# Performance work log

Measured on AMD Instinct MI355X. Metric: run time of the kernel, lower is better.

## Reference

```python
import jax, jax.numpy as jnp
import numpy as np

B, L, D, H, K_DELAYS = 8, 2048, 512, 8, 8
DH = D // H


def setup_inputs() -> dict:
    key = jax.random.key(0)
    ks = jax.random.split(key, 6)
    def lin_w(k):
        return 0.02 * jax.random.normal(k, (D, D), jnp.float32)
    return {
        "x_q":  jax.random.normal(ks[0], (B, L, D), jnp.float32),
        "x_kv": jax.random.normal(ks[1], (B, L, D), jnp.float32),
        "Wq": lin_w(ks[2]), "bq": jnp.zeros((D,), jnp.float32),
        "Wk": lin_w(ks[3]), "bk": jnp.zeros((D,), jnp.float32),
        "Wv": lin_w(ks[4]), "bv": jnp.zeros((D,), jnp.float32),
        "Wo": lin_w(ks[5]), "bo": jnp.zeros((D,), jnp.float32),
    }


def reference(x_q, x_kv, Wq, bq, Wk, bk, Wv, bv, Wo, bo):
    Bx, Lx, Dx = x_q.shape

    def proj(x, W, b):  # torch Linear: x @ W.T + b, then split heads -> [B,H,L,dh]
        return (x @ W.T + b).reshape(Bx, Lx, H, DH).transpose(0, 2, 1, 3)

    q = proj(x_q, Wq, bq)
    k = proj(x_kv, Wk, bk)
    v = proj(x_kv, Wv, bv)

    # FFT-based autocorrelation over the time axis (axis=2)
    qz = q - q.mean(axis=2, keepdims=True)
    kz = k - k.mean(axis=2, keepdims=True)
    Qf = jnp.fft.rfft(qz, axis=2)
    Kf = jnp.fft.rfft(kz, axis=2)
    corr = jnp.fft.irfft(Qf * jnp.conj(Kf), n=Lx, axis=2).mean(axis=-1)  # [B,H,L]
    # torch expands corr to [B,H,Lq,Lk] then means over Lq -> identical to corr
    score = corr

    K = min(K_DELAYS, Lx)
    vals, idx = jax.lax.top_k(score, K)                    # [B,H,K]
    w = vals / (vals.sum(axis=-1, keepdims=True) + 1e-12)
    w = jax.lax.stop_gradient(w)                           # .detach() in torch

    # circular shift by -delay == gather at (t + delay) mod L
    t = jnp.arange(Lx)
    pos = (t[None, None, None, :] + idx[..., None]) % Lx   # [B,H,K,L]
    v_sh = jnp.take_along_axis(v[:, :, None, :, :], pos[..., None], axis=3)  # [B,H,K,L,dh]
    out = jnp.einsum('bhk,bhkld->bhld', w, v_sh)           # weighted sum over delays

    out = out.transpose(0, 2, 1, 3).reshape(Bx, Lx, Dx)
    return out @ Wo.T + bo
```

## Files before the change

### kernel.cpp

```cpp
#include <hip/hip_runtime.h>
#include <math.h>

#define BB 8
#define LL 2048
#define DD 512
#define HH 8
#define DHH 64
#define KD 8
#define MM (BB*LL)

typedef _Float16 f16x2 __attribute__((ext_vector_type(2)));
typedef _Float16 f16x4 __attribute__((ext_vector_type(4)));
typedef _Float16 f16x8 __attribute__((ext_vector_type(8)));
typedef float    f32x4 __attribute__((ext_vector_type(4)));

__device__ inline void cvt8(const float* __restrict__ s, _Float16* hp, _Float16* lp) {
    const float4 a = *(const float4*)s;
    const float4 b = *(const float4*)(s + 4);
    const float v[8] = {a.x, a.y, a.z, a.w, b.x, b.y, b.z, b.w};
    f16x8 hi, lo;
#pragma unroll
    for (int j = 0; j < 8; j++) {
        const _Float16 h = (_Float16)v[j];
        hi[j] = h;
        lo[j] = (_Float16)((v[j] - (float)h) * 512.0f);
    }
    *(f16x8*)hp = hi;
    if (lp) *(f16x8*)lp = lo;
}

__global__ __launch_bounds__(256) void prep_x(const float* __restrict__ xq,
                                              const float* __restrict__ xkv,
                                              _Float16* __restrict__ Xq_h, _Float16* __restrict__ Xq_l,
                                              _Float16* __restrict__ Xkv_h, _Float16* __restrict__ Xkv_l) {
    const int g = blockIdx.x * 256 + threadIdx.x;
    const int which = g >> 20;
    const size_t idx = (size_t)(g & 1048575) * 8;
    const float* src = which ? xkv : xq;
    _Float16* dh = which ? Xkv_h : Xq_h;
    _Float16* dl = which ? Xkv_l : Xq_l;
    cvt8(src + idx, dh + idx, dl + idx);
}

__global__ __launch_bounds__(256) void prep_w(const float* __restrict__ Wq, const float* __restrict__ Wk,
                                              const float* __restrict__ Wv, const float* __restrict__ Wo,
                                              _Float16* __restrict__ Wq_h, _Float16* __restrict__ Wq_l,
                                              _Float16* __restrict__ Wk_h, _Float16* __restrict__ Wk_l,
                                              _Float16* __restrict__ Wv_h, _Float16* __restrict__ Wo_h) {
    const int g = blockIdx.x * 256 + threadIdx.x;
    const int which = g >> 15;
    const size_t idx = (size_t)(g & 32767) * 8;
    if (which == 0)      cvt8(Wq + idx, Wq_h + idx, Wq_l + idx);
    else if (which == 1) cvt8(Wk + idx, Wk_h + idx, Wk_l + idx);
    else if (which == 2) cvt8(Wv + idx, Wv_h + idx, nullptr);
    else                 cvt8(Wo + idx, Wo_h + idx, nullptr);
}

template<int NPROD, int MODE>
__global__ __launch_bounds__(256, 2) void gemm_f16(const _Float16* __restrict__ Ag,
                                                   const _Float16* __restrict__ Al_g,
                                                   const _Float16* __restrict__ Bg,
                                                   const _Float16* __restrict__ Bl_g,
                                                   const float* __restrict__ bias,
                                                   void* __restrict__ Cv) {
    __shared__ __align__(16) _Float16 lds[(NPROD == 3) ? 20480 : 10240];
    _Float16* Ah = lds;
    _Float16* Bh = lds + 5120;
    _Float16* Al = (NPROD == 3) ? lds + 10240 : lds;
    _Float16* Bl = (NPROD == 3) ? lds + 15360 : lds;

    const int t  = threadIdx.x;
    const int l0 = blockIdx.x;
    const int m0 = (((l0 >> 5) << 3) | (l0 & 7)) * 128;
    const int n0 = ((l0 >> 3) & 3) * 128;

    const int lrow = t >> 2;
    const int lcol = (t & 3) * 8;
    const int wave = t >> 6;
    const int lane = t & 63;
    const int wm   = (wave >> 1) * 64;
    const int wn   = (wave & 1) * 64;
    const int lm   = lane & 15;
    const int quad = lane >> 4;

    f32x4 acc0[4][4] = {};
    f32x4 acc1[4][4] = {};

    f16x8 pa[2], pb[2], pal[2], pbl[2];
#pragma unroll
    for (int p = 0; p < 2; p++) {
        pa[p] = *(const f16x8*)(Ag + (size_t)(m0 + p * 64 + lrow) * 512 + lcol);
        pb[p] = *(const f16x8*)(Bg + (size_t)(n0 + p * 64 + lrow) * 512 + lcol);
        if (NPROD == 3) {
            pal[p] = *(const f16x8*)(Al_g + (size_t)(m0 + p * 64 + lrow) * 512 + lcol);
            pbl[p] = *(const f16x8*)(Bl_g + (size_t)(n0 + p * 64 + lrow) * 512 + lcol);
        }
    }

    for (int k0 = 0; k0 < 512; k0 += 32) {
        __syncthreads();
#pragma unroll
        for (int p = 0; p < 2; p++) {
            const int row = p * 64 + lrow;
            *(f16x8*)&Ah[row * 40 + lcol] = pa[p];
            *(f16x8*)&Bh[row * 40 + lcol] = pb[p];
            if (NPROD == 3) {
                *(f16x8*)&Al[row * 40 + lcol] = pal[p];
                *(f16x8*)&Bl[row * 40 + lcol] = pbl[p];
            }
        }
        __syncthreads();

        if (k0 + 32 < 512) {
            const int kn = k0 + 32;
#pragma unroll
            for (int p = 0; p < 2; p++) {
                pa[p] = *(const f16x8*)(Ag + (size_t)(m0 + p * 64 + lrow) * 512 + kn + lcol);
                pb[p] = *(const f16x8*)(Bg + (size_t)(n0 + p * 64 + lrow) * 512 + kn + lcol);
                if (NPROD == 3) {
                    pal[p] = *(const f16x8*)(Al_g + (size_t)(m0 + p * 64 + lrow) * 512 + kn + lcol);
                    pbl[p] = *(const f16x8*)(Bl_g + (size_t)(n0 + p * 64 + lrow) * 512 + kn + lcol);
                }
            }
        }

        f16x8 afh[4], bf[4];
#pragma unroll
        for (int mt = 0; mt < 4; mt++)
            afh[mt] = *(f16x8*)&Ah[(wm + mt * 16 + lm) * 40 + quad * 8];
#pragma unroll
        for (int nt = 0; nt < 4; nt++)
            bf[nt] = *(f16x8*)&Bh[(wn + nt * 16 + lm) * 40 + quad * 8];

#pragma unroll
        for (int mt = 0; mt < 4; mt++)
#pragma unroll
            for (int nt = 0; nt < 4; nt++)
                acc0[mt][nt] = __builtin_amdgcn_mfma_f32_16x16x32_f16(afh[mt], bf[nt], acc0[mt][nt], 0, 0, 0);

        if (NPROD == 3) {
            f16x8 afl[4];
#pragma unroll
            for (int mt = 0; mt < 4; mt++)
                afl[mt] = *(f16x8*)&Al[(wm + mt * 16 + lm) * 40 + quad * 8];
#pragma unroll
            for (int mt = 0; mt < 4; mt++)
#pragma unroll
                for (int nt = 0; nt < 4; nt++)
                    acc1[mt][nt] = __builtin_amdgcn_mfma_f32_16x16x32_f16(afl[mt], bf[nt], acc1[mt][nt], 0, 0, 0);
#pragma unroll
            for (int nt = 0; nt < 4; nt++)
                bf[nt] = *(f16x8*)&Bl[(wn + nt * 16 + lm) * 40 + quad * 8];
#pragma unroll
            for (int mt = 0; mt < 4; mt++)
#pragma unroll
                for (int nt = 0; nt < 4; nt++)
                    acc1[mt][nt] = __builtin_amdgcn_mfma_f32_16x16x32_f16(afh[mt], bf[nt], acc1[mt][nt], 0, 0, 0);
        }
    }

#pragma unroll
    for (int mt = 0; mt < 4; mt++) {
#pragma unroll
        for (int nt = 0; nt < 4; nt++) {
            const int n = n0 + wn + nt * 16 + lm;
            const float bv = bias[n];
            float val[4];
#pragma unroll
            for (int r = 0; r < 4; r++) {
                val[r] = acc0[mt][nt][r] + bv;
                if (NPROD == 3) val[r] += acc1[mt][nt][r] * (1.0f / 512.0f);
            }
            const int mbase = m0 + wm + mt * 16 + quad * 4;
            const int b_idx = mbase >> 11;
            const int lbase = mbase & 2047;
            if (MODE == 0) {
                float* C = (float*)Cv;
#pragma unroll
                for (int r = 0; r < 4; r++) C[(size_t)(mbase + r) * 512 + n] = val[r];
            } else if (MODE == 1) {
                float* C = (float*)Cv;
                float4 pv = make_float4(val[0], val[1], val[2], val[3]);
                *(float4*)&C[((size_t)(b_idx * 512 + n)) * 2048 + lbase] = pv;
            } else {
                _Float16* C = (_Float16*)Cv;
#pragma unroll
                for (int r = 0; r < 4; r++)
                    C[(size_t)b_idx * 1048576 + (size_t)(n >> 6) * 131072
                      + (size_t)(lbase + r) * 64 + (n & 63)] = (_Float16)val[r];
            }
        }
    }
}

#define PADI(i) ((i) + ((((i) >> 5)) << 2))

__device__ inline float2 cmul2(float2 a, float2 w) {
    return make_float2(a.x * w.x - a.y * w.y, a.x * w.y + a.y * w.x);
}
__device__ inline float2 cadd2(float2 a, float2 b) { return make_float2(a.x + b.x, a.y + b.y); }
__device__ inline float2 csub2(float2 a, float2 b) { return make_float2(a.x - b.x, a.y - b.y); }

__global__ __launch_bounds__(256) void fft_fwd(const float* __restrict__ qT,
                                               const float* __restrict__ kT,
                                               float* __restrict__ specP) {
    const int blk = blockIdx.x;
    const int bh   = blk >> 3;
    const int part = blk & 7;
    const int t    = threadIdx.x;
    __shared__ float2 Zs[2300];
    __shared__ float2 Wt[1024];
    __shared__ float2 Pacc[2048];

#pragma unroll
    for (int s = 0; s < 4; s++) {
        const int j = t + s * 256;
        float sv, cv;
        __sincosf(2.0f * (float)M_PI * (float)j / 2048.0f, &sv, &cv);
        Wt[j] = make_float2(cv, -sv);
    }
#pragma unroll
    for (int s = 0; s < 8; s++) Pacc[t + 256 * s] = make_float2(0.0f, 0.0f);

    const int low5 = t & 31, hi3 = t >> 5;
    const int low2 = t & 3,  hi6 = t >> 2;

    for (int j8 = 0; j8 < 8; j8++) {
        const int seq = bh * 64 + part * 8 + j8;
        const float* qp = qT + (size_t)seq * 2048;
        const float* kp = kT + (size_t)seq * 2048;
        float2 z[8];
#pragma unroll
        for (int s = 0; s < 8; s++) z[s] = make_float2(qp[t + 256 * s], kp[t + 256 * s]);
        __syncthreads();

#pragma unroll
        for (int sp = 0; sp < 4; sp++) {
            float2 u = z[sp], v = z[sp + 4];
            z[sp]     = cadd2(u, v);
            z[sp + 4] = cmul2(csub2(u, v), Wt[t + 256 * sp]);
        }
#pragma unroll
        for (int base = 0; base < 8; base += 4)
#pragma unroll
            for (int q2 = 0; q2 < 2; q2++) {
                float2 u = z[base + q2], v = z[base + q2 + 2];
                z[base + q2]     = cadd2(u, v);
                z[base + q2 + 2] = cmul2(csub2(u, v), Wt[2 * (t + 256 * q2)]);
            }
        {
            const float2 w = Wt[4 * t];
#pragma unroll
            for (int e = 0; e < 8; e += 2) {
                float2 u = z[e], v = z[e + 1];
                z[e]     = cadd2(u, v);
                z[e + 1] = cmul2(csub2(u, v), w);
            }
        }

#pragma unroll
        for (int s = 0; s < 8; s++) Zs[PADI(t + 256 * s)] = z[s];
        __syncthreads();
#pragma unroll
        for (int s = 0; s < 8; s++) z[s] = Zs[PADI(low5 + 32 * s + 256 * hi3)];
        __syncthreads();

#pragma unroll
        for (int sp = 0; sp < 4; sp++) {
            float2 u = z[sp], v = z[sp + 4];
            z[sp]     = cadd2(u, v);
            z[sp + 4] = cmul2(csub2(u, v), Wt[8 * (low5 + 32 * sp)]);
        }
#pragma unroll
        for (int base = 0; base < 8; base += 4)
#pragma unroll
            for (int q2 = 0; q2 < 2; q2++) {
                float2 u = z[base + q2], v = z[base + q2 + 2];
                z[base + q2]     = cadd2(u, v);
                z[base + q2 + 2] = cmul2(csub2(u, v), Wt[16 * (low5 + 32 * q2)]);
            }
        {
            const float2 w = Wt[32 * low5];
#pragma unroll
            for (int e = 0; e < 8; e += 2) {
                float2 u = z[e], v = z[e + 1];
                z[e]     = cadd2(u, v);
                z[e + 1] = cmul2(csub2(u, v), w);
            }
        }

#pragma unroll
        for (int s = 0; s < 8; s++) Zs[PADI(low5 + 32 * s + 256 * hi3)] = z[s];
        __syncthreads();
#pragma unroll
        for (int s = 0; s < 8; s++) z[s] = Zs[PADI(low2 + 4 * s + 32 * hi6)];
        __syncthreads();

#pragma unroll
        for (int sp = 0; sp < 4; sp++) {
            float2 u = z[sp], v = z[sp + 4];
            z[sp]     = cadd2(u, v);
            z[sp + 4] = cmul2(csub2(u, v), Wt[64 * (low2 + 4 * sp)]);
        }
#pragma unroll
        for (int base = 0; base < 8; base += 4)
#pragma unroll
            for (int q2 = 0; q2 < 2; q2++) {
                float2 u = z[base + q2], v = z[base + q2 + 2];
                z[base + q2]     = cadd2(u, v);
                z[base + q2 + 2] = cmul2(csub2(u, v), Wt[128 * (low2 + 4 * q2)]);
            }
        {
            const float2 w = Wt[256 * low2];
#pragma unroll
            for (int e = 0; e < 8; e += 2) {
                float2 u = z[e], v = z[e + 1];
                z[e]     = cadd2(u, v);
                z[e + 1] = cmul2(csub2(u, v), w);
            }
        }

#pragma unroll
        for (int s = 0; s < 8; s++) Zs[PADI(low2 + 4 * s + 32 * hi6)] = z[s];
        __syncthreads();
#pragma unroll
        for (int s = 0; s < 8; s++) z[s] = Zs[PADI(8 * t + s)];
        __syncthreads();

#pragma unroll
        for (int base = 0; base < 8; base += 4) {
            {
                float2 u = z[base], v = z[base + 2];
                z[base]     = cadd2(u, v);
                z[base + 2] = csub2(u, v);
            }
            {
                float2 u = z[base + 1], v = z[base + 3];
                float2 d = csub2(u, v);
                z[base + 1] = cadd2(u, v);
                z[base + 3] = make_float2(d.y, -d.x);
            }
        }
#pragma unroll
        for (int e = 0; e < 8; e += 2) {
            float2 u = z[e], v = z[e + 1];
            z[e]     = cadd2(u, v);
            z[e + 1] = csub2(u, v);
        }

#pragma unroll
        for (int s = 0; s < 8; s++) Zs[8 * t + s] = z[s];
        __syncthreads();

#pragma unroll
        for (int s = 0; s < 8; s++) {
            const int p  = t + 256 * s;
            const int f  = (int)(__brev((unsigned)p) >> 21);
            const int fm = (2048 - f) & 2047;
            const int p2 = (int)(__brev((unsigned)fm) >> 21);
            const float2 zf = Zs[p];
            const float2 zm = Zs[p2];
            const float qr = 0.5f * (zf.x + zm.x);
            const float qi = 0.5f * (zf.y - zm.y);
            const float kr = 0.5f * (zf.y + zm.y);
            const float ki = 0.5f * (zm.x - zf.x);
            if (f != 0) {
                const float pr = qr * kr + qi * ki;
                const float pi = qi * kr - qr * ki;
                float2 acc = Pacc[p];
                Pacc[p] = make_float2(acc.x + pr, acc.y + pi);
            }
        }
        __syncthreads();
    }

    float2* outp = (float2*)specP + (size_t)blk * 2048;
#pragma unroll
    for (int s = 0; s < 8; s++) {
        const int p = t + 256 * s;
        outp[p] = Pacc[p];
    }
}

__device__ inline void build_twiddle(float2* Wt, int tid, float sign) {
#pragma unroll
    for (int s = 0; s < 4; s++) {
        const int j = tid + s * 256;
        const float a = 2.0f * (float)M_PI * (float)j / 2048.0f;
        float sv, cv;
        __sincosf(a, &sv, &cv);
        Wt[j] = make_float2(cv, sign * sv);
    }
}

__device__ inline void fft2048_stages(float2* Z, const float2* Wt, int tid) {
    for (int st = 0; st < 11; st++) {
        const int half = 1 << st;
        const int shift = 10 - st;
#pragma unroll
        for (int r = 0; r < 4; r++) {
            const int m   = tid + r * 256;
            const int grp = m >> st;
            const int pos = m & (half - 1);
            const int i0  = (grp << (st + 1)) + pos;
            const int i1  = i0 + half;
            const float2 w = Wt[pos << shift];
            const float2 a = Z[i0];
            const float2 b = Z[i1];
            const float tr = b.x * w.x - b.y * w.y;
            const float ti = b.x * w.y + b.y * w.x;
            Z[i0] = make_float2(a.x + tr, a.y + ti);
            Z[i1] = make_float2(a.x - tr, a.y - ti);
        }
        __syncthreads();
    }
}

__global__ __launch_bounds__(256) void fft_inv_topk(const float* __restrict__ specP,
                                                    int* __restrict__ delays,
                                                    float* __restrict__ weights) {
    const int bh  = blockIdx.x;
    const int tid = threadIdx.x;
    __shared__ float2 Z[2048];
    __shared__ float2 Wt[1024];
    __shared__ float  corrS[2048];
    __shared__ float  rv[256];
    __shared__ int    ri[256];
    __shared__ float  vals[KD];
    __shared__ int    inds[KD];

    build_twiddle(Wt, tid, +1.0f);

    const float2* sp = (const float2*)specP + (size_t)bh * 8 * 2048;
#pragma unroll
    for (int s = 0; s < 8; s++) {
        const int p = tid + s * 256;
        float2 acc = make_float2(0.0f, 0.0f);
#pragma unroll
        for (int part = 0; part < 8; part++) {
            const float2 v = sp[part * 2048 + p];
            acc.x += v.x; acc.y += v.y;
        }
        Z[p] = acc;
    }
    __syncthreads();
    fft2048_stages(Z, Wt, tid);

    const float scale = 1.0f / (2048.0f * 64.0f);
#pragma unroll
    for (int s = 0; s < 8; s++) {
        const int i = tid + s * 256;
        corrS[i] = Z[i].x * scale;
    }
    __syncthreads();

    for (int k = 0; k < KD; k++) {
        float best = -1e30f;
        int   bi   = 1 << 30;
        for (int i = tid; i < 2048; i += 256) {
            const float v = corrS[i];
            if (v > best || (v == best && i < bi)) { best = v; bi = i; }
        }
        rv[tid] = best;
        ri[tid] = bi;
        __syncthreads();
        for (int off = 128; off > 0; off >>= 1) {
            if (tid < off) {
                const float v2 = rv[tid + off];
                const int   i2 = ri[tid + off];
                if (v2 > rv[tid] || (v2 == rv[tid] && i2 < ri[tid])) {
                    rv[tid] = v2; ri[tid] = i2;
                }
            }
            __syncthreads();
        }
        if (tid == 0) {
            vals[k] = rv[0];
            inds[k] = ri[0];
            corrS[ri[0]] = -1e30f;
        }
        __syncthreads();
    }

    if (tid == 0) {
        float sum = 0.0f;
        for (int k = 0; k < KD; k++) sum += vals[k];
        const float inv = 1.0f / (sum + 1e-12f);
        for (int k = 0; k < KD; k++) {
            weights[bh * KD + k] = vals[k] * inv;
            delays[bh * KD + k]  = inds[k];
        }
    }
}

__global__ __launch_bounds__(256) void gather_ws(const _Float16* __restrict__ v,
                                                 const int* __restrict__ delays,
                                                 const float* __restrict__ weights,
                                                 _Float16* __restrict__ outb) {
    const int gp  = blockIdx.x * 256 + threadIdx.x;
    const int ch2 = gp & 255;
    const int m   = gp >> 8;
    const int l   = m & 2047;
    const int b   = m >> 11;
    const int ch  = ch2 * 2;
    const int h   = ch >> 6;
    const int dh  = ch & 63;
    const int bh  = b * 8 + h;

    const _Float16* vb = v + (size_t)bh * 131072;
    float a0 = 0.0f, a1 = 0.0f;
#pragma unroll
    for (int k = 0; k < KD; k++) {
        const int   d = delays[bh * KD + k];
        const float w = weights[bh * KD + k];
        const int   p = (l + d) & 2047;
        const f16x2 pv = *(const f16x2*)&vb[p * 64 + dh];
        a0 = fmaf(w, (float)pv[0], a0);
        a1 = fmaf(w, (float)pv[1], a1);
    }
    f16x2 ov;
    ov[0] = (_Float16)a0;
    ov[1] = (_Float16)a1;
    *(f16x2*)&outb[(size_t)m * 512 + ch] = ov;
}

extern "C" void kernel_launch(void* const* d_in, const int* in_sizes, int n_in,
                              void* d_out, int out_size, void* d_ws, size_t ws_size,
                              hipStream_t stream) {
    const float* x_q  = (const float*)d_in[0];
    const float* x_kv = (const float*)d_in[1];
    const float* Wq   = (const float*)d_in[2];
    const float* bq   = (const float*)d_in[3];
    const float* Wk   = (const float*)d_in[4];
    const float* bk   = (const float*)d_in[5];
    const float* Wv   = (const float*)d_in[6];
    const float* bv   = (const float*)d_in[7];
    const float* Wo   = (const float*)d_in[8];
    const float* bo   = (const float*)d_in[9];
    float* out = (float*)d_out;

    char* ws = (char*)d_ws;
    _Float16* Xq_h  = (_Float16*)(ws + 0);
    _Float16* Xq_l  = (_Float16*)(ws + 16777216);
    _Float16* Xkv_h = (_Float16*)(ws + 33554432);
    _Float16* Xkv_l = (_Float16*)(ws + 50331648);
    _Float16* Wq_h  = (_Float16*)(ws + 67108864);
    _Float16* Wq_l  = (_Float16*)(ws + 67633152);
    _Float16* Wk_h  = (_Float16*)(ws + 68157440);
    _Float16* Wk_l  = (_Float16*)(ws + 68681728);
    _Float16* Wv_h  = (_Float16*)(ws + 69206016);
    _Float16* Wo_h  = (_Float16*)(ws + 69730304);
    int*      dely  = (int*)    (ws + 70254592);
    float*    wgt   = (float*)  (ws + 70256640);
    float*    kf32  = (float*)  (ws + 0);
    float*    specP = (float*)  (ws + 50331648);
    _Float16* vh    = (_Float16*)(ws + 0);
    _Float16* gbuf  = (_Float16*)(ws + 16777216);
    float*    qf32  = (float*)d_out;

    dim3 blk(256);

    prep_x<<<dim3(8192), blk, 0, stream>>>(x_q, x_kv, Xq_h, Xq_l, Xkv_h, Xkv_l);
    prep_w<<<dim3(512),  blk, 0, stream>>>(Wq, Wk, Wv, Wo, Wq_h, Wq_l, Wk_h, Wk_l, Wv_h, Wo_h);

    gemm_f16<3, 1><<<dim3(512), blk, 0, stream>>>(Xq_h,  Xq_l,  Wq_h, Wq_l, bq, qf32);
    gemm_f16<3, 1><<<dim3(512), blk, 0, stream>>>(Xkv_h, Xkv_l, Wk_h, Wk_l, bk, kf32);

    fft_fwd<<<dim3(512), blk, 0, stream>>>(qf32, kf32, specP);
    fft_inv_topk<<<dim3(BB * HH), blk, 0, stream>>>(specP, dely, wgt);

    gemm_f16<1, 2><<<dim3(512), blk, 0, stream>>>(Xkv_h, Xkv_h, Wv_h, Wv_h, bv, vh);

    gather_ws<<<dim3(MM * 256 / 256), blk, 0, stream>>>(vh, dely, wgt, gbuf);

    gemm_f16<1, 0><<<dim3(512), blk, 0, stream>>>(gbuf, gbuf, Wo_h, Wo_h, bo, out);
}
```

Baseline: 304.1 us.

## Merge prep kernels, split FFT across more blocks, widen gather vectors

The two fp16 conversion kernels are merged into one launch. The forward FFT now uses 16 blocks per batch-head instead of 8, which doubles parallelism. It keeps the partial spectrum accumulator in registers instead of LDS, drops the trailing barriers after each LDS read, and switches to a different padding scheme for the shared buffer. The inverse kernel sums over 16 partial spectra, and the gather kernel processes 4 channels per thread with 8-byte loads and stores. Together these aim to cut launch overhead, barrier count and memory instructions, at the cost of more partial-spectrum traffic and more inverse-side reduction.

```diff
diff --git a/kernel.cpp b/kernel.cpp
--- a/kernel.cpp
+++ b/kernel.cpp
@@ -29,31 +29,33 @@
     if (lp) *(f16x8*)lp = lo;
 }
 
-__global__ __launch_bounds__(256) void prep_x(const float* __restrict__ xq,
-                                              const float* __restrict__ xkv,
-                                              _Float16* __restrict__ Xq_h, _Float16* __restrict__ Xq_l,
-                                              _Float16* __restrict__ Xkv_h, _Float16* __restrict__ Xkv_l) {
-    const int g = blockIdx.x * 256 + threadIdx.x;
-    const int which = g >> 20;
-    const size_t idx = (size_t)(g & 1048575) * 8;
-    const float* src = which ? xkv : xq;
-    _Float16* dh = which ? Xkv_h : Xq_h;
-    _Float16* dl = which ? Xkv_l : Xq_l;
-    cvt8(src + idx, dh + idx, dl + idx);
-}
-
-__global__ __launch_bounds__(256) void prep_w(const float* __restrict__ Wq, const float* __restrict__ Wk,
-                                              const float* __restrict__ Wv, const float* __restrict__ Wo,
-                                              _Float16* __restrict__ Wq_h, _Float16* __restrict__ Wq_l,
-                                              _Float16* __restrict__ Wk_h, _Float16* __restrict__ Wk_l,
-                                              _Float16* __restrict__ Wv_h, _Float16* __restrict__ Wo_h) {
-    const int g = blockIdx.x * 256 + threadIdx.x;
-    const int which = g >> 15;
-    const size_t idx = (size_t)(g & 32767) * 8;
-    if (which == 0)      cvt8(Wq + idx, Wq_h + idx, Wq_l + idx);
-    else if (which == 1) cvt8(Wk + idx, Wk_h + idx, Wk_l + idx);
-    else if (which == 2) cvt8(Wv + idx, Wv_h + idx, nullptr);
-    else                 cvt8(Wo + idx, Wo_h + idx, nullptr);
+__global__ __launch_bounds__(256) void prep_all(const float* __restrict__ xq,
+                                                const float* __restrict__ xkv,
+                                                const float* __restrict__ Wq, const float* __restrict__ Wk,
+                                                const float* __restrict__ Wv, const float* __restrict__ Wo,
+                                                _Float16* __restrict__ Xq_h, _Float16* __restrict__ Xq_l,
+                                                _Float16* __restrict__ Xkv_h, _Float16* __restrict__ Xkv_l,
+                                                _Float16* __restrict__ Wq_h, _Float16* __restrict__ Wq_l,
+                                                _Float16* __restrict__ Wk_h, _Float16* __restrict__ Wk_l,
+                                                _Float16* __restrict__ Wv_h, _Float16* __restrict__ Wo_h) {
+    const int bid = blockIdx.x;
+    if (bid < 8192) {
+        const int g = bid * 256 + threadIdx.x;
+        const int which = g >> 20;
+        const size_t idx = (size_t)(g & 1048575) * 8;
+        const float* src = which ? xkv : xq;
+        _Float16* dh = which ? Xkv_h : Xq_h;
+        _Float16* dl = which ? Xkv_l : Xq_l;
+        cvt8(src + idx, dh + idx, dl + idx);
+    } else {
+        const int g = (bid - 8192) * 256 + threadIdx.x;
+        const int which = g >> 15;
+        const size_t idx = (size_t)(g & 32767) * 8;
+        if (which == 0)      cvt8(Wq + idx, Wq_h + idx, Wq_l + idx);
+        else if (which == 1) cvt8(Wk + idx, Wk_h + idx, Wk_l + idx);
+        else if (which == 2) cvt8(Wv + idx, Wv_h + idx, nullptr);
+        else                 cvt8(Wo + idx, Wo_h + idx, nullptr);
+    }
 }
 
 template<int NPROD, int MODE>
@@ -193,7 +195,7 @@
     }
 }
 
-#define PADI(i) ((i) + ((((i) >> 5)) << 2))
+#define PAD3(i) ((i) + ((i) >> 3))
 
 __device__ inline float2 cmul2(float2 a, float2 w) {
     return make_float2(a.x * w.x - a.y * w.y, a.x * w.y + a.y * w.x);
@@ -204,13 +206,12 @@
 __global__ __launch_bounds__(256) void fft_fwd(const float* __restrict__ qT,
                                                const float* __restrict__ kT,
                                                float* __restrict__ specP) {
-    const int blk = blockIdx.x;
-    const int bh   = blk >> 3;
-    const int part = blk & 7;
+    const int blk  = blockIdx.x;
+    const int bh   = blk >> 4;
+    const int part = blk & 15;
     const int t    = threadIdx.x;
-    __shared__ float2 Zs[2300];
+    __shared__ float2 Zs[2304];
     __shared__ float2 Wt[1024];
-    __shared__ float2 Pacc[2048];
 
 #pragma unroll
     for (int s = 0; s < 4; s++) {
@@ -219,14 +220,16 @@
         __sincosf(2.0f * (float)M_PI * (float)j / 2048.0f, &sv, &cv);
         Wt[j] = make_float2(cv, -sv);
     }
-#pragma unroll
-    for (int s = 0; s < 8; s++) Pacc[t + 256 * s] = make_float2(0.0f, 0.0f);
+
+    float2 pacc[8];
+#pragma unroll
+    for (int s = 0; s < 8; s++) pacc[s] = make_float2(0.0f, 0.0f);
 
     const int low5 = t & 31, hi3 = t >> 5;
     const int low2 = t & 3,  hi6 = t >> 2;
 
-    for (int j8 = 0; j8 < 8; j8++) {
-        const int seq = bh * 64 + part * 8 + j8;
+    for (int j4 = 0; j4 < 4; j4++) {
+        const int seq = bh * 64 + part * 4 + j4;
         const float* qp = qT + (size_t)seq * 2048;
         const float* kp = kT + (size_t)seq * 2048;
         float2 z[8];
@@ -259,11 +262,10 @@
         }
 
 #pragma unroll
-        for (int s = 0; s < 8; s++) Zs[PADI(t + 256 * s)] = z[s];
-        __syncthreads();
-#pragma unroll
-        for (int s = 0; s < 8; s++) z[s] = Zs[PADI(low5 + 32 * s + 256 * hi3)];
-        __syncthreads();
+        for (int s = 0; s < 8; s++) Zs[PAD3(t + 256 * s)] = z[s];
+        __syncthreads();
+#pragma unroll
+        for (int s = 0; s < 8; s++) z[s] = Zs[PAD3(low5 + 32 * s + 256 * hi3)];
 
 #pragma unroll
         for (int sp = 0; sp < 4; sp++) {
@@ -290,11 +292,10 @@
         }
 
 #pragma unroll
-        for (int s = 0; s < 8; s++) Zs[PADI(low5 + 32 * s + 256 * hi3)] = z[s];
-        __syncthreads();
-#pragma unroll
-        for (int s = 0; s < 8; s++) z[s] = Zs[PADI(low2 + 4 * s + 32 * hi6)];
-        __syncthreads();
+        for (int s = 0; s < 8; s++) Zs[PAD3(low5 + 32 * s + 256 * hi3)] = z[s];
+        __syncthreads();
+#pragma unroll
+        for (int s = 0; s < 8; s++) z[s] = Zs[PAD3(low2 + 4 * s + 32 * hi6)];
 
 #pragma unroll
         for (int sp = 0; sp < 4; sp++) {
@@ -321,11 +322,10 @@
         }
 
 #pragma unroll
-        for (int s = 0; s < 8; s++) Zs[PADI(low2 + 4 * s + 32 * hi6)] = z[s];
-        __syncthreads();
-#pragma unroll
-        for (int s = 0; s < 8; s++) z[s] = Zs[PADI(8 * t + s)];
-        __syncthreads();
+        for (int s = 0; s < 8; s++) Zs[PAD3(low2 + 4 * s + 32 * hi6)] = z[s];
+        __syncthreads();
+#pragma unroll
+        for (int s = 0; s < 8; s++) z[s] = Zs[PAD3(8 * t + s)];
 
 #pragma unroll
         for (int base = 0; base < 8; base += 4) {
@@ -349,7 +349,7 @@
         }
 
 #pragma unroll
-        for (int s = 0; s < 8; s++) Zs[8 * t + s] = z[s];
+        for (int s = 0; s < 8; s++) Zs[PAD3(8 * t + s)] = z[s];
         __syncthreads();
 
 #pragma unroll
@@ -358,28 +358,22 @@
             const int f  = (int)(__brev((unsigned)p) >> 21);
             const int fm = (2048 - f) & 2047;
             const int p2 = (int)(__brev((unsigned)fm) >> 21);
-            const float2 zf = Zs[p];
-            const float2 zm = Zs[p2];
+            const float2 zf = Zs[PAD3(p)];
+            const float2 zm = Zs[PAD3(p2)];
             const float qr = 0.5f * (zf.x + zm.x);
             const float qi = 0.5f * (zf.y - zm.y);
             const float kr = 0.5f * (zf.y + zm.y);
             const float ki = 0.5f * (zm.x - zf.x);
             if (f != 0) {
-                const float pr = qr * kr + qi * ki;
-                const float pi = qi * kr - qr * ki;
-                float2 acc = Pacc[p];
-                Pacc[p] = make_float2(acc.x + pr, acc.y + pi);
-            }
-        }
-        __syncthreads();
+                pacc[s].x += qr * kr + qi * ki;
+                pacc[s].y += qi * kr - qr * ki;
+            }
+        }
     }
 
     float2* outp = (float2*)specP + (size_t)blk * 2048;
 #pragma unroll
-    for (int s = 0; s < 8; s++) {
-        const int p = t + 256 * s;
-        outp[p] = Pacc[p];
-    }
+    for (int s = 0; s < 8; s++) outp[t + 256 * s] = pacc[s];
 }
 
 __device__ inline void build_twiddle(float2* Wt, int tid, float sign) {
@@ -431,13 +425,13 @@
 
     build_twiddle(Wt, tid, +1.0f);
 
-    const float2* sp = (const float2*)specP + (size_t)bh * 8 * 2048;
+    const float2* sp = (const float2*)specP + (size_t)bh * 16 * 2048;
 #pragma unroll
     for (int s = 0; s < 8; s++) {
         const int p = tid + s * 256;
         float2 acc = make_float2(0.0f, 0.0f);
 #pragma unroll
-        for (int part = 0; part < 8; part++) {
+        for (int part = 0; part < 16; part++) {
             const float2 v = sp[part * 2048 + p];
             acc.x += v.x; acc.y += v.y;
         }
@@ -497,31 +491,35 @@
                                                  const int* __restrict__ delays,
                                                  const float* __restrict__ weights,
                                                  _Float16* __restrict__ outb) {
-    const int gp  = blockIdx.x * 256 + threadIdx.x;
-    const int ch2 = gp & 255;
-    const int m   = gp >> 8;
-    const int l   = m & 2047;
-    const int b   = m >> 11;
-    const int ch  = ch2 * 2;
-    const int h   = ch >> 6;
-    const int dh  = ch & 63;
-    const int bh  = b * 8 + h;
+    const int gp = blockIdx.x * 256 + threadIdx.x;
+    const int c4 = gp & 127;
+    const int m  = gp >> 7;
+    const int l  = m & 2047;
+    const int b  = m >> 11;
+    const int ch = c4 * 4;
+    const int h  = ch >> 6;
+    const int dh = ch & 63;
+    const int bh = b * 8 + h;
 
     const _Float16* vb = v + (size_t)bh * 131072;
-    float a0 = 0.0f, a1 = 0.0f;
+    float a0 = 0.0f, a1 = 0.0f, a2 = 0.0f, a3 = 0.0f;
 #pragma unroll
     for (int k = 0; k < KD; k++) {
         const int   d = delays[bh * KD + k];
         const float w = weights[bh * KD + k];
         const int   p = (l + d) & 2047;
-        const f16x2 pv = *(const f16x2*)&vb[p * 64 + dh];
+        const f16x4 pv = *(const f16x4*)&vb[p * 64 + dh];
         a0 = fmaf(w, (float)pv[0], a0);
         a1 = fmaf(w, (float)pv[1], a1);
-    }
-    f16x2 ov;
+        a2 = fmaf(w, (float)pv[2], a2);
+        a3 = fmaf(w, (float)pv[3], a3);
+    }
+    f16x4 ov;
     ov[0] = (_Float16)a0;
     ov[1] = (_Float16)a1;
-    *(f16x2*)&outb[(size_t)m * 512 + ch] = ov;
+    ov[2] = (_Float16)a2;
+    ov[3] = (_Float16)a3;
+    *(f16x4*)&outb[(size_t)m * 512 + ch] = ov;
 }
 
 extern "C" void kernel_launch(void* const* d_in, const int* in_sizes, int n_in,
@@ -560,18 +558,19 @@
 
     dim3 blk(256);
 
-    prep_x<<<dim3(8192), blk, 0, stream>>>(x_q, x_kv, Xq_h, Xq_l, Xkv_h, Xkv_l);
-    prep_w<<<dim3(512),  blk, 0, stream>>>(Wq, Wk, Wv, Wo, Wq_h, Wq_l, Wk_h, Wk_l, Wv_h, Wo_h);
+    prep_all<<<dim3(8704), blk, 0, stream>>>(x_q, x_kv, Wq, Wk, Wv, Wo,
+                                             Xq_h, Xq_l, Xkv_h, Xkv_l,
+                                             Wq_h, Wq_l, Wk_h, Wk_l, Wv_h, Wo_h);
 
     gemm_f16<3, 1><<<dim3(512), blk, 0, stream>>>(Xq_h,  Xq_l,  Wq_h, Wq_l, bq, qf32);
     gemm_f16<3, 1><<<dim3(512), blk, 0, stream>>>(Xkv_h, Xkv_l, Wk_h, Wk_l, bk, kf32);
 
-    fft_fwd<<<dim3(512), blk, 0, stream>>>(qf32, kf32, specP);
+    fft_fwd<<<dim3(1024), blk, 0, stream>>>(qf32, kf32, specP);
     fft_inv_topk<<<dim3(BB * HH), blk, 0, stream>>>(specP, dely, wgt);
 
     gemm_f16<1, 2><<<dim3(512), blk, 0, stream>>>(Xkv_h, Xkv_h, Wv_h, Wv_h, bv, vh);
 
-    gather_ws<<<dim3(MM * 256 / 256), blk, 0, stream>>>(vh, dely, wgt, gbuf);
+    gather_ws<<<dim3(8192), blk, 0, stream>>>(vh, dely, wgt, gbuf);
 
     gemm_f16<1, 0><<<dim3(512), blk, 0, stream>>>(gbuf, gbuf, Wo_h, Wo_h, bo, out);
 }
```

After: 301.0 us. No clear change (-1.0%).
